# Kernel tuning notes

Hardware: AMD Instinct MI355X
Metric: run time of the kernel (lower is better)

Reference implementation:

```python
import jax, jax.numpy as jnp
import numpy as np

NUM_EXPERTS = 8
DIM = 1024
HIDDEN = 2048
N_TOKENS = 8192  # rows of x, includes padding beyond sum(num_tokens_per_expert)


def setup_inputs() -> dict:
    key = jax.random.key(0)
    k_x, k_w1, k_w2, k_w3 = jax.random.split(key, 4)
    x = jax.random.normal(k_x, (N_TOKENS, DIM), dtype=jnp.float32)
    # trunc_normal(std=0.02)-like init; w2 is zeros in torch init but we use
    w1 = jax.random.normal(k_w1, (NUM_EXPERTS, HIDDEN, DIM), dtype=jnp.float32) * 0.02
    w2 = jax.random.normal(k_w2, (NUM_EXPERTS, DIM, HIDDEN), dtype=jnp.float32) * 0.02
    w3 = jax.random.normal(k_w3, (NUM_EXPERTS, HIDDEN, DIM), dtype=jnp.float32) * 0.02
    # routed token counts per expert; sum <= N_TOKENS, remainder is padding
    num_tokens_per_expert = jnp.array([995, 1000, 980, 1010, 970, 1020, 990, 1005], dtype=jnp.int64)
    return {"x": x, "num_tokens_per_expert": num_tokens_per_expert,
            "w1": w1, "w2": w2, "w3": w3}


def reference(x, num_tokens_per_expert, w1, w2, w3):
    # Mirrors torch _run_experts_for_loop with act='silu'. The torch code calls
    # .tolist() on the counts (shapes are data-dependent), so we likewise treat
    # the per-expert counts as static host values.
    counts = np.asarray(num_tokens_per_expert).astype(np.int64)
    offsets = np.concatenate([np.zeros(1, np.int64), np.cumsum(counts)])
    total = int(offsets[-1])
    num_experts = w1.shape[0]
    out_splits = []
    for e in range(num_experts):
        xe = x[int(offsets[e]):int(offsets[e + 1])]            # [n_e, dim]
        gate = jax.nn.silu(xe @ w1[e].T)                       # [n_e, hidden]
        h = gate * (xe @ w3[e].T)                              # SwiGLU
        out_splits.append(h @ w2[e].T)                         # [n_e, dim]
    out = jnp.concatenate(out_splits, axis=0)
    num_padding = x.shape[0] - total
    if num_padding > 0:
        out = jnp.concatenate([out, jnp.zeros((num_padding, out.shape[-1]), out.dtype)], axis=0)
    return out
```

## Files before the change

### kernel.cpp

```cpp
#include <hip/hip_runtime.h>

#define NEXP 8
#define DIM  1024
#define HID  2048
#define NTOK 8192

#define BM 128
#define BN 128
#define BK 32
#define LDK 40

typedef short s16x8 __attribute__((ext_vector_type(8)));
typedef float f32x4 __attribute__((ext_vector_type(4)));
typedef unsigned short u16;

__device__ __forceinline__ u16 f2bf(float f) {
  unsigned int u = __builtin_bit_cast(unsigned int, f);
  u += 0x7FFFu + ((u >> 16) & 1u);
  return (u16)(u >> 16);
}

__device__ __forceinline__ void gload16(const u16* g, u16* l) {
  __builtin_amdgcn_global_load_lds((const __attribute__((address_space(1))) void*)g,
                                   (__attribute__((address_space(3))) void*)l, 16, 0, 0);
}

__device__ __forceinline__ bool find_tile(const int* __restrict__ cnts, int rt,
                                          int& e_out, int& row0, int& cnt_out, long long& off_out) {
  long long off = 0; int cum = 0;
  #pragma unroll
  for (int e = 0; e < NEXP; ++e) {
    int c = cnts[e];
    int nt = (c + BM - 1) / BM;
    if (rt < cum + nt) { e_out = e; row0 = (rt - cum) * BM; cnt_out = c; off_out = off; return true; }
    cum += nt; off += c;
  }
  return false;
}

__global__ __launch_bounds__(256) void cvt_kernel(const float* __restrict__ in,
                                                  u16* __restrict__ out, int n8) {
  for (int i = blockIdx.x * blockDim.x + threadIdx.x; i < n8; i += gridDim.x * blockDim.x) {
    const float4* p = (const float4*)in + 2 * (size_t)i;
    const float4 a = p[0], b = p[1];
    s16x8 v;
    v[0] = (short)f2bf(a.x); v[1] = (short)f2bf(a.y); v[2] = (short)f2bf(a.z); v[3] = (short)f2bf(a.w);
    v[4] = (short)f2bf(b.x); v[5] = (short)f2bf(b.y); v[6] = (short)f2bf(b.z); v[7] = (short)f2bf(b.w);
    *((s16x8*)out + (size_t)i) = v;
  }
}

#define XSTR 68
__global__ __launch_bounds__(512, 4) void gemm1_bf16(
    const u16* __restrict__ xb, const int* __restrict__ cnts,
    const u16* __restrict__ w1b, const u16* __restrict__ w3b,
    u16* __restrict__ hbuf)
{
  int e, row0, cnt; long long off;
  if (!find_tile(cnts, blockIdx.y, e, row0, cnt, off)) return;
  const int ct = blockIdx.x;

  __shared__ float smem_f[4 * 64 * XSTR];
  u16* As  = (u16*)smem_f;
  u16* B1s = As + BM * BK;
  u16* B3s = As + 2 * BM * BK;

  const int t    = threadIdx.x;
  const int lane = t & 63;
  const int wid  = t >> 6;
  const int mat  = wid >> 2;
  const int sw   = wid & 3;
  const int wr = sw >> 1, wc = sw & 1;
  const int lr = lane & 15;
  const int lk = (lane >> 4) * 8;

  const u16* xrow = xb + (size_t)(off + row0) * DIM;
  const u16* w1t  = w1b + ((size_t)e * HID + (size_t)ct * BN) * DIM;
  const u16* w3t  = w3b + ((size_t)e * HID + (size_t)ct * BN) * DIM;

  f32x4 acc[4][4];
  const f32x4 zf = {0.f, 0.f, 0.f, 0.f};
  #pragma unroll
  for (int i = 0; i < 4; ++i)
    #pragma unroll
    for (int j = 0; j < 4; ++j) acc[i][j] = zf;

  const int sidx = wid * 512 + lane * 8;
  const int srow = sidx >> 5;
  const int scol = sidx & 31;

  const u16* Bsel = mat ? B3s : B1s;

  for (int k0 = 0; k0 < DIM; k0 += BK) {
    __syncthreads();
    {
      const size_t go = (size_t)srow * DIM + k0 + scol;
      gload16(&xrow[go], As  + wid * 512);
      gload16(&w1t [go], B1s + wid * 512);
      gload16(&w3t [go], B3s + wid * 512);
    }
    __syncthreads();

    s16x8 af[4], bf[4];
    #pragma unroll
    for (int fm = 0; fm < 4; ++fm)
      af[fm] = *(const s16x8*)&As[(wr * 64 + fm * 16 + lr) * BK + lk];
    #pragma unroll
    for (int fn = 0; fn < 4; ++fn)
      bf[fn] = *(const s16x8*)&Bsel[(wc * 64 + fn * 16 + lr) * BK + lk];
    #pragma unroll
    for (int fm = 0; fm < 4; ++fm)
      #pragma unroll
      for (int fn = 0; fn < 4; ++fn)
        acc[fm][fn] = __builtin_amdgcn_mfma_f32_16x16x32_bf16(af[fm], bf[fn], acc[fm][fn], 0, 0, 0);
  }

  __syncthreads();
  if (mat) {
    float* up = smem_f + sw * (64 * XSTR);
    #pragma unroll
    for (int fm = 0; fm < 4; ++fm)
      #pragma unroll
      for (int fn = 0; fn < 4; ++fn)
        #pragma unroll
        for (int j = 0; j < 4; ++j)
          up[(fm * 16 + ((lane >> 4) << 2) + j) * XSTR + fn * 16 + lr] = acc[fm][fn][j];
  }
  __syncthreads();
  if (!mat) {
    const float* up = smem_f + sw * (64 * XSTR);
    #pragma unroll
    for (int fm = 0; fm < 4; ++fm)
      #pragma unroll
      for (int fn = 0; fn < 4; ++fn) {
        const int col = ct * BN + wc * 64 + fn * 16 + lr;
        #pragma unroll
        for (int j = 0; j < 4; ++j) {
          const int r = wr * 64 + fm * 16 + ((lane >> 4) << 2) + j;
          if (row0 + r < cnt) {
            const float gv = acc[fm][fn][j];
            const float uv = up[(fm * 16 + ((lane >> 4) << 2) + j) * XSTR + fn * 16 + lr];
            const float hv = (gv / (1.f + __expf(-gv))) * uv;
            hbuf[(size_t)(off + row0 + r) * HID + col] = f2bf(hv);
          }
        }
      }
  }
}

__global__ __launch_bounds__(256) void gemm2_bf16(
    const u16* __restrict__ hbuf, const int* __restrict__ cnts,
    const u16* __restrict__ w2b, float* __restrict__ out)
{
  int e, row0, cnt; long long off;
  if (!find_tile(cnts, blockIdx.y, e, row0, cnt, off)) return;
  const int ct = blockIdx.x;

  __shared__ u16 As[BM * BK];
  __shared__ u16 Bs[BN * BK];

  const int t    = threadIdx.x;
  const int lane = t & 63;
  const int wid  = t >> 6;
  const int wr = wid >> 1, wc = wid & 1;
  const int lr = lane & 15;
  const int lk = (lane >> 4) * 8;

  const u16* arow = hbuf + (size_t)(off + row0) * HID;
  const u16* w2t  = w2b + ((size_t)e * DIM + (size_t)ct * BN) * HID;

  f32x4 acc[4][4];
  const f32x4 zf = {0.f, 0.f, 0.f, 0.f};
  #pragma unroll
  for (int i = 0; i < 4; ++i)
    #pragma unroll
    for (int j = 0; j < 4; ++j) acc[i][j] = zf;

  for (int k0 = 0; k0 < HID; k0 += BK) {
    __syncthreads();
    #pragma unroll
    for (int c = 0; c < 2; ++c) {
      const int chunk = wid * 2 + c;
      const int idx   = chunk * 512 + lane * 8;
      const int r  = idx >> 5;
      const int cc = idx & 31;
      const size_t go = (size_t)r * HID + k0 + cc;
      gload16(&arow[go], &As[chunk * 512]);
      gload16(&w2t [go], &Bs[chunk * 512]);
    }
    __syncthreads();

    s16x8 af[4], bf[4];
    #pragma unroll
    for (int fm = 0; fm < 4; ++fm)
      af[fm] = *(const s16x8*)&As[(wr * 64 + fm * 16 + lr) * BK + lk];
    #pragma unroll
    for (int fn = 0; fn < 4; ++fn)
      bf[fn] = *(const s16x8*)&Bs[(wc * 64 + fn * 16 + lr) * BK + lk];
    #pragma unroll
    for (int fm = 0; fm < 4; ++fm)
      #pragma unroll
      for (int fn = 0; fn < 4; ++fn)
        acc[fm][fn] = __builtin_amdgcn_mfma_f32_16x16x32_bf16(af[fm], bf[fn], acc[fm][fn], 0, 0, 0);
  }

  #pragma unroll
  for (int fm = 0; fm < 4; ++fm)
    #pragma unroll
    for (int fn = 0; fn < 4; ++fn) {
      const int col = ct * BN + wc * 64 + fn * 16 + lr;
      #pragma unroll
      for (int j = 0; j < 4; ++j) {
        const int r = wr * 64 + fm * 16 + ((lane >> 4) << 2) + j;
        if (row0 + r < cnt)
          out[(size_t)(off + row0 + r) * DIM + col] = acc[fm][fn][j];
      }
    }
}

__global__ __launch_bounds__(256) void gemm1_kernel(
    const float* __restrict__ x, const int* __restrict__ cnts,
    const float* __restrict__ w1, const float* __restrict__ w3,
    u16* __restrict__ hbuf)
{
  int e, row0, cnt; long long off;
  if (!find_tile(cnts, blockIdx.y, e, row0, cnt, off)) return;
  const int ct = blockIdx.x;

  __shared__ u16 As [BM * LDK];
  __shared__ u16 B1s[BN * LDK];
  __shared__ u16 B3s[BN * LDK];

  const int t    = threadIdx.x;
  const int srow = t >> 3;
  const int skq  = (t & 7) * 4;
  const int lane = t & 63;
  const int wid  = t >> 6;
  const int wr = wid >> 1, wc = wid & 1;
  const int lr = lane & 15;
  const int lk = (lane >> 4) * 8;

  const float* w1e = w1 + (size_t)e * HID * DIM;
  const float* w3e = w3 + (size_t)e * HID * DIM;

  f32x4 accg[4][4], accu[4][4];
  const f32x4 zf = {0.f, 0.f, 0.f, 0.f};
  #pragma unroll
  for (int i = 0; i < 4; ++i)
    #pragma unroll
    for (int j = 0; j < 4; ++j) { accg[i][j] = zf; accu[i][j] = zf; }

  for (int k0 = 0; k0 < DIM; k0 += BK) {
    __syncthreads();
    #pragma unroll
    for (int s = 0; s < 4; ++s) {
      const int r = s * 32 + srow;
      float4 va = make_float4(0.f, 0.f, 0.f, 0.f);
      const int gm = row0 + r;
      if (gm < cnt) va = *(const float4*)&x[(size_t)(off + gm) * DIM + k0 + skq];
      ushort4 ua; ua.x = f2bf(va.x); ua.y = f2bf(va.y); ua.z = f2bf(va.z); ua.w = f2bf(va.w);
      *(ushort4*)&As[r * LDK + skq] = ua;
      const size_t gb = (size_t)(ct * BN + r) * DIM + k0 + skq;
      const float4 v1 = *(const float4*)&w1e[gb];
      const float4 v3 = *(const float4*)&w3e[gb];
      ushort4 u1; u1.x = f2bf(v1.x); u1.y = f2bf(v1.y); u1.z = f2bf(v1.z); u1.w = f2bf(v1.w);
      ushort4 u3; u3.x = f2bf(v3.x); u3.y = f2bf(v3.y); u3.z = f2bf(v3.z); u3.w = f2bf(v3.w);
      *(ushort4*)&B1s[r * LDK + skq] = u1;
      *(ushort4*)&B3s[r * LDK + skq] = u3;
    }
    __syncthreads();

    s16x8 af[4], b1f[4], b3f[4];
    #pragma unroll
    for (int fm = 0; fm < 4; ++fm)
      af[fm] = *(const s16x8*)&As[(wr * 64 + fm * 16 + lr) * LDK + lk];
    #pragma unroll
    for (int fn = 0; fn < 4; ++fn) {
      b1f[fn] = *(const s16x8*)&B1s[(wc * 64 + fn * 16 + lr) * LDK + lk];
      b3f[fn] = *(const s16x8*)&B3s[(wc * 64 + fn * 16 + lr) * LDK + lk];
    }
    #pragma unroll
    for (int fm = 0; fm < 4; ++fm)
      #pragma unroll
      for (int fn = 0; fn < 4; ++fn) {
        accg[fm][fn] = __builtin_amdgcn_mfma_f32_16x16x32_bf16(af[fm], b1f[fn], accg[fm][fn], 0, 0, 0);
        accu[fm][fn] = __builtin_amdgcn_mfma_f32_16x16x32_bf16(af[fm], b3f[fn], accu[fm][fn], 0, 0, 0);
      }
  }

  #pragma unroll
  for (int fm = 0; fm < 4; ++fm)
    #pragma unroll
    for (int fn = 0; fn < 4; ++fn) {
      const f32x4 g = accg[fm][fn], u = accu[fm][fn];
      const int col = ct * BN + wc * 64 + fn * 16 + lr;
      #pragma unroll
      for (int j = 0; j < 4; ++j) {
        const int r = wr * 64 + fm * 16 + ((lane >> 4) << 2) + j;
        if (row0 + r < cnt) {
          const float gv = g[j];
          const float hv = (gv / (1.f + __expf(-gv))) * u[j];
          hbuf[(size_t)(off + row0 + r) * HID + col] = f2bf(hv);
        }
      }
    }
}

__global__ __launch_bounds__(256) void gemm2_kernel(
    const u16* __restrict__ hbuf, const int* __restrict__ cnts,
    const float* __restrict__ w2, float* __restrict__ out)
{
  int e, row0, cnt; long long off;
  if (!find_tile(cnts, blockIdx.y, e, row0, cnt, off)) return;
  const int ct = blockIdx.x;

  __shared__ u16 As[BM * LDK];
  __shared__ u16 Bs[BN * LDK];

  const int t    = threadIdx.x;
  const int srow = t >> 3;
  const int skq  = (t & 7) * 4;
  const int lane = t & 63;
  const int wid  = t >> 6;
  const int wr = wid >> 1, wc = wid & 1;
  const int lr = lane & 15;
  const int lk = (lane >> 4) * 8;

  const float* w2e = w2 + (size_t)e * DIM * HID;

  f32x4 acc[4][4];
  const f32x4 zf = {0.f, 0.f, 0.f, 0.f};
  #pragma unroll
  for (int i = 0; i < 4; ++i)
    #pragma unroll
    for (int j = 0; j < 4; ++j) acc[i][j] = zf;

  for (int k0 = 0; k0 < HID; k0 += BK) {
    __syncthreads();
    #pragma unroll
    for (int s = 0; s < 4; ++s) {
      const int r = s * 32 + srow;
      ushort4 ua = make_ushort4(0, 0, 0, 0);
      const int gm = row0 + r;
      if (gm < cnt) ua = *(const ushort4*)&hbuf[(size_t)(off + gm) * HID + k0 + skq];
      *(ushort4*)&As[r * LDK + skq] = ua;
      const float4 v2 = *(const float4*)&w2e[(size_t)(ct * BN + r) * HID + k0 + skq];
      ushort4 u2; u2.x = f2bf(v2.x); u2.y = f2bf(v2.y); u2.z = f2bf(v2.z); u2.w = f2bf(v2.w);
      *(ushort4*)&Bs[r * LDK + skq] = u2;
    }
    __syncthreads();

    s16x8 af[4], bf[4];
    #pragma unroll
    for (int fm = 0; fm < 4; ++fm)
      af[fm] = *(const s16x8*)&As[(wr * 64 + fm * 16 + lr) * LDK + lk];
    #pragma unroll
    for (int fn = 0; fn < 4; ++fn)
      bf[fn] = *(const s16x8*)&Bs[(wc * 64 + fn * 16 + lr) * LDK + lk];
    #pragma unroll
    for (int fm = 0; fm < 4; ++fm)
      #pragma unroll
      for (int fn = 0; fn < 4; ++fn)
        acc[fm][fn] = __builtin_amdgcn_mfma_f32_16x16x32_bf16(af[fm], bf[fn], acc[fm][fn], 0, 0, 0);
  }

  #pragma unroll
  for (int fm = 0; fm < 4; ++fm)
    #pragma unroll
    for (int fn = 0; fn < 4; ++fn) {
      const int col = ct * BN + wc * 64 + fn * 16 + lr;
      #pragma unroll
      for (int j = 0; j < 4; ++j) {
        const int r = wr * 64 + fm * 16 + ((lane >> 4) << 2) + j;
        if (row0 + r < cnt)
          out[(size_t)(off + row0 + r) * DIM + col] = acc[fm][fn][j];
      }
    }
}

__global__ void zero_pad_kernel(const int* __restrict__ cnts, float* __restrict__ out)
{
  int total = 0;
  #pragma unroll
  for (int e = 0; e < NEXP; ++e) total += cnts[e];
  const int row = blockIdx.x;
  if (row < total) return;
  float4* p = (float4*)(out + (size_t)row * DIM);
  p[threadIdx.x] = make_float4(0.f, 0.f, 0.f, 0.f);
}

extern "C" void kernel_launch(void* const* d_in, const int* in_sizes, int n_in,
                              void* d_out, int out_size, void* d_ws, size_t ws_size,
                              hipStream_t stream) {
  const float* x    = (const float*)d_in[0];
  const int*   cnts = (const int*)d_in[1];
  const float* w1   = (const float*)d_in[2];
  const float* w2   = (const float*)d_in[3];
  const float* w3   = (const float*)d_in[4];
  float*       out  = (float*)d_out;

  const size_t HBUF_E = (size_t)NTOK * HID;
  const size_t XB_E   = (size_t)NTOK * DIM;
  const size_t W_E    = (size_t)NEXP * HID * DIM;
  const size_t need   = (HBUF_E + XB_E + 2 * W_E) * sizeof(u16);

  u16* hbuf = (u16*)d_ws;
  dim3 blk(256);

  if (ws_size >= need) {
    u16* xb = hbuf + HBUF_E;
    u16* wA = xb + XB_E;
    u16* wB = wA + W_E;

    cvt_kernel<<<dim3(2048), blk, 0, stream>>>(x,  xb, (int)(XB_E / 8));
    cvt_kernel<<<dim3(2048), blk, 0, stream>>>(w1, wA, (int)(W_E / 8));
    cvt_kernel<<<dim3(2048), blk, 0, stream>>>(w3, wB, (int)(W_E / 8));
    gemm1_bf16<<<dim3(HID / BN, 72), dim3(512), 0, stream>>>(xb, cnts, wA, wB, hbuf);
    cvt_kernel<<<dim3(2048), blk, 0, stream>>>(w2, wA, (int)(W_E / 8));
    gemm2_bf16<<<dim3(DIM / BN, 72), blk, 0, stream>>>(hbuf, cnts, wA, out);
  } else {
    gemm1_kernel<<<dim3(HID / BN, 72), blk, 0, stream>>>(x, cnts, w1, w3, hbuf);
    gemm2_kernel<<<dim3(DIM / BN, 72), blk, 0, stream>>>(hbuf, cnts, w2, out);
  }
  zero_pad_kernel<<<dim3(NTOK), dim3(256), 0, stream>>>(cnts, out);
}
```

Baseline: 213.2 us.

## Double-buffer LDS staging in both GEMMs and fuse conversion launches

Both bf16 GEMM kernels now use two LDS stage buffers: the next K tile is loaded asynchronously while the current tile is fed to MFMA, with one barrier per iteration instead of two. The separate fp32-to-bf16 conversion launches are merged into one multi-array kernel, and when workspace allows, w2 is converted up front into its own buffer. This aims to hide global-load latency behind compute and cut launch overhead, at the cost of more LDS per block in gemm2 and more workspace.

```diff
diff --git a/kernel.cpp b/kernel.cpp
--- a/kernel.cpp
+++ b/kernel.cpp
@@ -38,15 +38,26 @@
   return false;
 }
 
-__global__ __launch_bounds__(256) void cvt_kernel(const float* __restrict__ in,
-                                                  u16* __restrict__ out, int n8) {
-  for (int i = blockIdx.x * blockDim.x + threadIdx.x; i < n8; i += gridDim.x * blockDim.x) {
-    const float4* p = (const float4*)in + 2 * (size_t)i;
-    const float4 a = p[0], b = p[1];
-    s16x8 v;
-    v[0] = (short)f2bf(a.x); v[1] = (short)f2bf(a.y); v[2] = (short)f2bf(a.z); v[3] = (short)f2bf(a.w);
-    v[4] = (short)f2bf(b.x); v[5] = (short)f2bf(b.y); v[6] = (short)f2bf(b.z); v[7] = (short)f2bf(b.w);
-    *((s16x8*)out + (size_t)i) = v;
+__device__ __forceinline__ void cvt8(const float* __restrict__ s, u16* __restrict__ d, int j) {
+  const float4* p = (const float4*)s + 2 * (size_t)j;
+  const float4 a = p[0], b = p[1];
+  s16x8 v;
+  v[0] = (short)f2bf(a.x); v[1] = (short)f2bf(a.y); v[2] = (short)f2bf(a.z); v[3] = (short)f2bf(a.w);
+  v[4] = (short)f2bf(b.x); v[5] = (short)f2bf(b.y); v[6] = (short)f2bf(b.z); v[7] = (short)f2bf(b.w);
+  *((s16x8*)d + (size_t)j) = v;
+}
+
+__global__ __launch_bounds__(256) void cvt_multi(
+    const float* __restrict__ s0, u16* __restrict__ d0, int n0,
+    const float* __restrict__ s1, u16* __restrict__ d1, int n1,
+    const float* __restrict__ s2, u16* __restrict__ d2, int n2,
+    const float* __restrict__ s3, u16* __restrict__ d3, int n3) {
+  const int b0 = n0, b1 = b0 + n1, b2 = b1 + n2, b3 = b2 + n3;
+  for (int i = blockIdx.x * blockDim.x + threadIdx.x; i < b3; i += gridDim.x * blockDim.x) {
+    if      (i < b0) cvt8(s0, d0, i);
+    else if (i < b1) cvt8(s1, d1, i - b0);
+    else if (i < b2) cvt8(s2, d2, i - b1);
+    else             cvt8(s3, d3, i - b2);
   }
 }
 
@@ -61,9 +72,7 @@
   const int ct = blockIdx.x;
 
   __shared__ float smem_f[4 * 64 * XSTR];
-  u16* As  = (u16*)smem_f;
-  u16* B1s = As + BM * BK;
-  u16* B3s = As + 2 * BM * BK;
+  u16* stage = (u16*)smem_f;
 
   const int t    = threadIdx.x;
   const int lane = t & 63;
@@ -89,33 +98,40 @@
   const int srow = sidx >> 5;
   const int scol = sidx & 31;
 
-  const u16* Bsel = mat ? B3s : B1s;
-
-  for (int k0 = 0; k0 < DIM; k0 += BK) {
-    __syncthreads();
-    {
-      const size_t go = (size_t)srow * DIM + k0 + scol;
-      gload16(&xrow[go], As  + wid * 512);
-      gload16(&w1t [go], B1s + wid * 512);
-      gload16(&w3t [go], B3s + wid * 512);
-    }
-    __syncthreads();
-
+  auto STAGE = [&](int k0, int b) {
+    u16* base = stage + b * (3 * 4096);
+    const size_t go = (size_t)srow * DIM + k0 + scol;
+    gload16(&xrow[go], base        + wid * 512);
+    gload16(&w1t [go], base + 4096 + wid * 512);
+    gload16(&w3t [go], base + 8192 + wid * 512);
+  };
+
+  STAGE(0, 0);
+  __syncthreads();
+  int cur = 0;
+  const int NT = DIM / BK;
+  for (int kt = 0; kt < NT; ++kt) {
+    if (kt + 1 < NT) STAGE((kt + 1) * BK, cur ^ 1);
+
+    const u16* Asb = stage + cur * (3 * 4096);
+    const u16* Bsb = Asb + 4096 + mat * 4096;
     s16x8 af[4], bf[4];
     #pragma unroll
     for (int fm = 0; fm < 4; ++fm)
-      af[fm] = *(const s16x8*)&As[(wr * 64 + fm * 16 + lr) * BK + lk];
+      af[fm] = *(const s16x8*)&Asb[(wr * 64 + fm * 16 + lr) * BK + lk];
     #pragma unroll
     for (int fn = 0; fn < 4; ++fn)
-      bf[fn] = *(const s16x8*)&Bsel[(wc * 64 + fn * 16 + lr) * BK + lk];
+      bf[fn] = *(const s16x8*)&Bsb[(wc * 64 + fn * 16 + lr) * BK + lk];
     #pragma unroll
     for (int fm = 0; fm < 4; ++fm)
       #pragma unroll
       for (int fn = 0; fn < 4; ++fn)
         acc[fm][fn] = __builtin_amdgcn_mfma_f32_16x16x32_bf16(af[fm], bf[fn], acc[fm][fn], 0, 0, 0);
-  }
-
-  __syncthreads();
+
+    __syncthreads();
+    cur ^= 1;
+  }
+
   if (mat) {
     float* up = smem_f + sw * (64 * XSTR);
     #pragma unroll
@@ -156,8 +172,7 @@
   if (!find_tile(cnts, blockIdx.y, e, row0, cnt, off)) return;
   const int ct = blockIdx.x;
 
-  __shared__ u16 As[BM * BK];
-  __shared__ u16 Bs[BN * BK];
+  __shared__ u16 stage[2 * 2 * BM * BK];
 
   const int t    = threadIdx.x;
   const int lane = t & 63;
@@ -176,8 +191,8 @@
     #pragma unroll
     for (int j = 0; j < 4; ++j) acc[i][j] = zf;
 
-  for (int k0 = 0; k0 < HID; k0 += BK) {
-    __syncthreads();
+  auto STAGE = [&](int k0, int b) {
+    u16* base = stage + b * (2 * 4096);
     #pragma unroll
     for (int c = 0; c < 2; ++c) {
       const int chunk = wid * 2 + c;
@@ -185,23 +200,35 @@
       const int r  = idx >> 5;
       const int cc = idx & 31;
       const size_t go = (size_t)r * HID + k0 + cc;
-      gload16(&arow[go], &As[chunk * 512]);
-      gload16(&w2t [go], &Bs[chunk * 512]);
-    }
-    __syncthreads();
-
+      gload16(&arow[go], base        + chunk * 512);
+      gload16(&w2t [go], base + 4096 + chunk * 512);
+    }
+  };
+
+  STAGE(0, 0);
+  __syncthreads();
+  int cur = 0;
+  const int NT = HID / BK;
+  for (int kt = 0; kt < NT; ++kt) {
+    if (kt + 1 < NT) STAGE((kt + 1) * BK, cur ^ 1);
+
+    const u16* Asb = stage + cur * (2 * 4096);
+    const u16* Bsb = Asb + 4096;
     s16x8 af[4], bf[4];
     #pragma unroll
     for (int fm = 0; fm < 4; ++fm)
-      af[fm] = *(const s16x8*)&As[(wr * 64 + fm * 16 + lr) * BK + lk];
+      af[fm] = *(const s16x8*)&Asb[(wr * 64 + fm * 16 + lr) * BK + lk];
     #pragma unroll
     for (int fn = 0; fn < 4; ++fn)
-      bf[fn] = *(const s16x8*)&Bs[(wc * 64 + fn * 16 + lr) * BK + lk];
+      bf[fn] = *(const s16x8*)&Bsb[(wc * 64 + fn * 16 + lr) * BK + lk];
     #pragma unroll
     for (int fm = 0; fm < 4; ++fm)
       #pragma unroll
       for (int fn = 0; fn < 4; ++fn)
         acc[fm][fn] = __builtin_amdgcn_mfma_f32_16x16x32_bf16(af[fm], bf[fn], acc[fm][fn], 0, 0, 0);
+
+    __syncthreads();
+    cur ^= 1;
   }
 
   #pragma unroll
@@ -402,21 +429,30 @@
   const size_t HBUF_E = (size_t)NTOK * HID;
   const size_t XB_E   = (size_t)NTOK * DIM;
   const size_t W_E    = (size_t)NEXP * HID * DIM;
-  const size_t need   = (HBUF_E + XB_E + 2 * W_E) * sizeof(u16);
+  const size_t need_min  = (HBUF_E + XB_E + 2 * W_E) * sizeof(u16);
+  const size_t need_full = (HBUF_E + XB_E + 3 * W_E) * sizeof(u16);
 
   u16* hbuf = (u16*)d_ws;
   dim3 blk(256);
-
-  if (ws_size >= need) {
+  const int XB8 = (int)(XB_E / 8), W8 = (int)(W_E / 8);
+
+  if (ws_size >= need_full) {
     u16* xb = hbuf + HBUF_E;
     u16* wA = xb + XB_E;
     u16* wB = wA + W_E;
-
-    cvt_kernel<<<dim3(2048), blk, 0, stream>>>(x,  xb, (int)(XB_E / 8));
-    cvt_kernel<<<dim3(2048), blk, 0, stream>>>(w1, wA, (int)(W_E / 8));
-    cvt_kernel<<<dim3(2048), blk, 0, stream>>>(w3, wB, (int)(W_E / 8));
+    u16* wC = wB + W_E;
+    cvt_multi<<<dim3(2048), blk, 0, stream>>>(x, xb, XB8, w1, wA, W8, w3, wB, W8, w2, wC, W8);
     gemm1_bf16<<<dim3(HID / BN, 72), dim3(512), 0, stream>>>(xb, cnts, wA, wB, hbuf);
-    cvt_kernel<<<dim3(2048), blk, 0, stream>>>(w2, wA, (int)(W_E / 8));
+    gemm2_bf16<<<dim3(DIM / BN, 72), blk, 0, stream>>>(hbuf, cnts, wC, out);
+  } else if (ws_size >= need_min) {
+    u16* xb = hbuf + HBUF_E;
+    u16* wA = xb + XB_E;
+    u16* wB = wA + W_E;
+    cvt_multi<<<dim3(2048), blk, 0, stream>>>(x, xb, XB8, w1, wA, W8, w3, wB, W8, (const float*)nullptr, (u16*)nullptr, 0);
+    gemm1_bf16<<<dim3(HID / BN, 72), dim3(512), 0, stream>>>(xb, cnts, wA, wB, hbuf);
+    cvt_multi<<<dim3(2048), blk, 0, stream>>>(w2, wA, W8, (const float*)nullptr, (u16*)nullptr, 0,
+                                              (const float*)nullptr, (u16*)nullptr, 0,
+                                              (const float*)nullptr, (u16*)nullptr, 0);
     gemm2_bf16<<<dim3(DIM / BN, 72), blk, 0, stream>>>(hbuf, cnts, wA, out);
   } else {
     gemm1_kernel<<<dim3(HID / BN, 72), blk, 0, stream>>>(x, cnts, w1, w3, hbuf);
```

Result: faster. 205.4 us (-3.7%).
